# Performance work log

Hardware: AMD Instinct MI355X
Metric: run time of the kernel (lower is better)

## Reference

```python
import jax, jax.numpy as jnp
import numpy as np

B, C, H, W = 32, 3, 128, 128
OH, OW = 32, 32
N = OH * OW


def calc_mask(mu_x, mu_y, sigma_x, sigma_y):
    # Gaussian receptive-field mask, normalized per neuron over (C,H,W) and
    # rescaled by sqrt(C*H*W), as in AdaptiveLocal2DLayer.calc_U (channel_separate=False,
    # normed=True). The mask is identical across channels, so we keep it [H,W,N]
    # and fold the channel count C into the normalization.
    xg = jnp.linspace(0.0, 1.0, W)
    yg = jnp.linspace(0.0, 1.0, H)
    gx = jnp.exp(-0.5 * ((xg[:, None] - mu_x[None, :]) / sigma_x[None, :]) ** 2)  # [W,N]
    gy = jnp.exp(-0.5 * ((yg[:, None] - mu_y[None, :]) / sigma_y[None, :]) ** 2)  # [H,N]
    g = gy[:, None, :] * gx[None, :, :]  # [H,W,N]
    sumsq = C * jnp.sum(g * g, axis=(0, 1), keepdims=True)  # per-neuron sum over C,H,W
    return g / jnp.sqrt(sumsq) * jnp.sqrt(jnp.asarray(C * H * W, dtype=g.dtype))


def setup_inputs() -> dict:
    key = jax.random.key(0)
    kx, kw = jax.random.split(key)
    x = jax.random.normal(kx, (B, C, H, W), dtype=jnp.float32)
    # mu_init='spread': grid of centers with margin 0.2 (np.meshgrid default 'xy')
    margin = 0.2
    grid_y, grid_x = jnp.meshgrid(
        jnp.linspace(margin, 1.0 - margin, OH),
        jnp.linspace(margin, 1.0 - margin, OW),
        indexing='xy')
    mu_x = grid_x.flatten().astype(jnp.float32)
    mu_y = grid_y.flatten().astype(jnp.float32)
    sigma_x = jnp.full((N,), 0.1, dtype=jnp.float32)
    sigma_y = jnp.full((N,), 0.1, dtype=jnp.float32)
    # weight init as in the module: uniform(-bound, bound) with
    # bound = gain*sqrt(6/(eff_fan_in + fan_out)), eff_fan_in = sum(mask^2)
    mask = calc_mask(mu_x, mu_y, sigma_x, sigma_y)
    eff_fan_in = C * jnp.sum(mask ** 2)
    gain = float(np.sqrt(2.0))  # calculate_gain('relu')
    bound = gain * jnp.sqrt(6.0 / (eff_fan_in + N))
    weights = jax.random.uniform(kw, (C, H, W, N), minval=-bound, maxval=bound,
                                 dtype=jnp.float32)
    return {"x": x, "mu_x": mu_x, "mu_y": mu_y,
            "sigma_x": sigma_x, "sigma_y": sigma_y, "weights": weights}


def reference(x, mu_x, mu_y, sigma_x, sigma_y, weights):
    # forward: weighted_mask = mask * weights; tensordot over (C,H,W)
    mask = calc_mask(mu_x, mu_y, sigma_x, sigma_y)  # [H,W,N]
    wm = mask[None, :, :, :] * weights               # [C,H,W,N]
    out = jnp.einsum('bchw,chwn->bn', x, wm)         # [B,N]
    return out.reshape(x.shape[0], 1, OH, OW)
```

## Files before the change

kernel.cpp:

```cpp
#include <hip/hip_runtime.h>

#define BB 32
#define CC 3
#define HH 128
#define WW 128
#define NN 1024
#define KK (CC*HH*WW)
#define NROWS (CC*HH)
#define KSR NROWS
#define BH 16
#define NSL 512
#define WCH 4
#define NCH (WW/WCH)
#define SG 8
#define STEP (1.0f/127.0f)

__global__ void scale_kernel(const float* __restrict__ mu_x,
                             const float* __restrict__ mu_y,
                             const float* __restrict__ sigma_x,
                             const float* __restrict__ sigma_y,
                             float* __restrict__ scale) {
    int n = blockIdx.x * blockDim.x + threadIdx.x;
    if (n >= NN) return;
    float mux = mu_x[n], muy = mu_y[n];
    float isx = 1.0f / sigma_x[n], isy = 1.0f / sigma_y[n];
    float Sx = 0.f, Sy = 0.f;
    for (int i = 0; i < WW; ++i) {
        float dx = (i * STEP - mux) * isx;
        Sx += __expf(-dx * dx);
        float dy = (i * STEP - muy) * isy;
        Sy += __expf(-dy * dy);
    }
    scale[n] = sqrtf((float)(HH * WW) / (Sx * Sy));
}

__global__ void xpose_kernel(const float* __restrict__ x, float* __restrict__ xT) {
    __shared__ float tile[64][BB + 1];
    int k0 = blockIdx.x * 64;
    int lane = threadIdx.x & 63;
    int bgrp = threadIdx.x >> 6;
#pragma unroll
    for (int i = 0; i < 8; ++i) {
        int b = bgrp * 8 + i;
        tile[lane][b] = x[(size_t)b * KK + k0 + lane];
    }
    __syncthreads();
    int b = threadIdx.x & 31;
    int kk0 = threadIdx.x >> 5;
#pragma unroll
    for (int i = 0; i < 8; ++i) {
        int kk = i * 8 + kk0;
        xT[(size_t)(k0 + kk) * BB + b] = tile[kk][b];
    }
}

__global__ __launch_bounds__(256) void main_pipe(
    const float* __restrict__ weights,
    const float* __restrict__ xT,
    const float* __restrict__ scale,
    const float* __restrict__ mu_x, const float* __restrict__ mu_y,
    const float* __restrict__ sigma_x, const float* __restrict__ sigma_y,
    float* __restrict__ part)
{
    const int tid = threadIdx.x;

    const int d    = blockIdx.x;
    const int xcd  = d & 7;
    const int slot = d >> 3;
    const int g    = xcd * (KSR / 8) + (slot >> 2);
    const int sib  = slot & 3;
    const int b0   = (sib & 1) * BH;
    const int nh   = sib >> 1;
    const int r    = g;
    const int h    = r & (HH - 1);
    const int np   = nh * 256 + tid;

    const float2 mux2 = ((const float2*)mu_x)[np];
    const float2 sx2  = ((const float2*)sigma_x)[np];
    const float2 muy2 = ((const float2*)mu_y)[np];
    const float2 sy2  = ((const float2*)sigma_y)[np];
    const float2 sc2  = ((const float2*)scale)[np];

    float mux[2] = {mux2.x, mux2.y};
    float ax[2], axs[2], Bf[2], gyrow[2];
    ax[0] = -0.5f/(sx2.x*sx2.x); ax[1] = -0.5f/(sx2.y*sx2.y);
    axs[0] = ax[0]*STEP;         axs[1] = ax[1]*STEP;
    Bf[0] = __expf(2.f*axs[0]*STEP); Bf[1] = __expf(2.f*axs[1]*STEP);
    {
        const float hp = h * STEP;
        float ayc, dd;
        ayc = -0.5f/(sy2.x*sy2.x); dd = hp-muy2.x; gyrow[0] = __expf(ayc*dd*dd)*sc2.x;
        ayc = -0.5f/(sy2.y*sy2.y); dd = hp-muy2.y; gyrow[1] = __expf(ayc*dd*dd)*sc2.y;
    }

    const float* wbase = weights + (size_t)r * WW * NN + np * 2;
    const float4* xr4  = (const float4*)xT + (size_t)r * (WW * BB / 4) + (b0 >> 2);

    float2 wR[2][4];
#define WLOAD(BUF, C)                                                   \
    {                                                                   \
        _Pragma("unroll")                                               \
        for (int i = 0; i < 4; ++i)                                     \
            wR[BUF][i] = *(const float2*)(wbase + (size_t)((C)*WCH + i) * NN); \
    }

    float2 acc[BH];
#pragma unroll
    for (int b = 0; b < BH; ++b) acc[b] = make_float2(0.f, 0.f);

    float g2[2], r2[2];
    auto resync = [&](int w0) {
        const float w0s = (float)w0 * STEP;
#pragma unroll
        for (int j = 0; j < 2; ++j) {
            const float dd = w0s - mux[j];
            g2[j] = __expf(ax[j] * dd * dd) * gyrow[j];
            r2[j] = __expf(axs[j] * (2.f * dd + STEP));
        }
    };

#define FMAQ(XC, B)                                                     \
    {                                                                   \
        acc[B].x = fmaf(XC, t0, acc[B].x);                              \
        acc[B].y = fmaf(XC, t1, acc[B].y);                              \
    }

#define CHUNK(BUF, C)                                                   \
    {                                                                   \
        if (((C) & 3) == 0) resync((C) * WCH);                          \
        _Pragma("unroll")                                               \
        for (int i = 0; i < 4; ++i) {                                   \
            const int w = (C) * WCH + i;                                \
            const float4 xq0 = xr4[w*8 + 0];                            \
            const float4 xq1 = xr4[w*8 + 1];                            \
            const float4 xq2 = xr4[w*8 + 2];                            \
            const float4 xq3 = xr4[w*8 + 3];                            \
            const float t0 = g2[0] * wR[BUF][i].x;                      \
            const float t1 = g2[1] * wR[BUF][i].y;                      \
            FMAQ(xq0.x,  0) FMAQ(xq0.y,  1) FMAQ(xq0.z,  2) FMAQ(xq0.w,  3) \
            FMAQ(xq1.x,  4) FMAQ(xq1.y,  5) FMAQ(xq1.z,  6) FMAQ(xq1.w,  7) \
            FMAQ(xq2.x,  8) FMAQ(xq2.y,  9) FMAQ(xq2.z, 10) FMAQ(xq2.w, 11) \
            FMAQ(xq3.x, 12) FMAQ(xq3.y, 13) FMAQ(xq3.z, 14) FMAQ(xq3.w, 15) \
            g2[0] *= r2[0]; g2[1] *= r2[1];                             \
            r2[0] *= Bf[0]; r2[1] *= Bf[1];                             \
        }                                                               \
    }

    WLOAD(0, 0);
    for (int c = 0; c < NCH; c += 2) {
        WLOAD(1, c + 1);
        CHUNK(0, c);
        if (c + 2 < NCH) WLOAD(0, c + 2);
        CHUNK(1, c + 1);
    }
#undef CHUNK
#undef FMAQ
#undef WLOAD

    float* pp = part + ((size_t)g * BB + b0) * NN + np * 2;
#pragma unroll
    for (int b = 0; b < BH; ++b)
        *(float2*)(pp + (size_t)b * NN) = acc[b];
}

__global__ __launch_bounds__(256) void reduce1_kernel(const float* __restrict__ part,
                                                      float* __restrict__ part2) {
    const int sg = blockIdx.x >> 5;
    const int cq = (blockIdx.x & 31) * 256 + threadIdx.x;
    const int s0 = sg * (KSR / SG);
    float4 a = make_float4(0.f, 0.f, 0.f, 0.f);
#pragma unroll 4
    for (int s = 0; s < KSR / SG; ++s) {
        const float4 v = *(const float4*)(part + (size_t)(s0 + s) * (BB * NN) + cq * 4);
        a.x += v.x; a.y += v.y; a.z += v.z; a.w += v.w;
    }
    *(float4*)(part2 + ((size_t)sg * (BB * NN) + cq * 4)) = a;
}

__global__ __launch_bounds__(256) void reduce2_kernel(const float* __restrict__ part2,
                                                      float* __restrict__ out) {
    const int cq = blockIdx.x * 256 + threadIdx.x;
    float4 a = make_float4(0.f, 0.f, 0.f, 0.f);
#pragma unroll
    for (int sgi = 0; sgi < SG; ++sgi) {
        const float4 v = *(const float4*)(part2 + (size_t)sgi * (BB * NN) + cq * 4);
        a.x += v.x; a.y += v.y; a.z += v.z; a.w += v.w;
    }
    *(float4*)(out + cq * 4) = a;
}

__global__ __launch_bounds__(256) void main_fallback(
    const float* __restrict__ weights,
    const float* __restrict__ x,
    const float* __restrict__ mu_x, const float* __restrict__ mu_y,
    const float* __restrict__ sigma_x, const float* __restrict__ sigma_y,
    float* __restrict__ dst)
{
    __shared__ float tile[2][WW][8];
    const int tid = threadIdx.x;
    const int g   = blockIdx.x;
    const int b0  = blockIdx.y * 8;
    const int r0  = g * 2;

    {
        const int b = tid & 7;
        const int c = tid >> 3;
        const float* xp = x + (size_t)(b0 + b) * KK + (size_t)r0 * WW + c * 8;
        const float4 v0 = ((const float4*)xp)[0];
        const float4 v1 = ((const float4*)xp)[1];
        const int row = (c * 8) >> 7;
        const int w   = (c * 8) & (WW - 1);
        tile[row][w+0][b] = v0.x; tile[row][w+1][b] = v0.y;
        tile[row][w+2][b] = v0.z; tile[row][w+3][b] = v0.w;
        tile[row][w+4][b] = v1.x; tile[row][w+5][b] = v1.y;
        tile[row][w+6][b] = v1.z; tile[row][w+7][b] = v1.w;
    }

    float4 mux4 = ((const float4*)mu_x)[tid];
    float4 muy4 = ((const float4*)mu_y)[tid];
    float4 sx4  = ((const float4*)sigma_x)[tid];
    float4 sy4  = ((const float4*)sigma_y)[tid];
    float4 ax4, ay4, sc4;
    ax4.x=-0.5f/(sx4.x*sx4.x); ax4.y=-0.5f/(sx4.y*sx4.y);
    ax4.z=-0.5f/(sx4.z*sx4.z); ax4.w=-0.5f/(sx4.w*sx4.w);
    ay4.x=-0.5f/(sy4.x*sy4.x); ay4.y=-0.5f/(sy4.y*sy4.y);
    ay4.z=-0.5f/(sy4.z*sy4.z); ay4.w=-0.5f/(sy4.w*sy4.w);
    {
        float Sx[4]={0,0,0,0}, Sy[4]={0,0,0,0};
        for (int i = 0; i < WW; ++i) {
            float pp = i * STEP, dd;
            dd=pp-mux4.x; Sx[0]+=__expf(2.f*ax4.x*dd*dd);
            dd=pp-mux4.y; Sx[1]+=__expf(2.f*ax4.y*dd*dd);
            dd=pp-mux4.z; Sx[2]+=__expf(2.f*ax4.z*dd*dd);
            dd=pp-mux4.w; Sx[3]+=__expf(2.f*ax4.w*dd*dd);
            dd=pp-muy4.x; Sy[0]+=__expf(2.f*ay4.x*dd*dd);
            dd=pp-muy4.y; Sy[1]+=__expf(2.f*ay4.y*dd*dd);
            dd=pp-muy4.z; Sy[2]+=__expf(2.f*ay4.z*dd*dd);
            dd=pp-muy4.w; Sy[3]+=__expf(2.f*ay4.w*dd*dd);
        }
        sc4.x = sqrtf((float)(HH*WW)/(Sx[0]*Sy[0]));
        sc4.y = sqrtf((float)(HH*WW)/(Sx[1]*Sy[1]));
        sc4.z = sqrtf((float)(HH*WW)/(Sx[2]*Sy[2]));
        sc4.w = sqrtf((float)(HH*WW)/(Sx[3]*Sy[3]));
    }
    __syncthreads();

    float acc[8][4];
#pragma unroll
    for (int b = 0; b < 8; ++b)
        acc[b][0] = acc[b][1] = acc[b][2] = acc[b][3] = 0.f;

#pragma unroll
    for (int rr = 0; rr < 2; ++rr) {
        const int rrow = r0 + rr;
        const int hh = rrow & (HH - 1);
        float4 gys;
        {
            float hp = hh * STEP, dd;
            dd=hp-muy4.x; gys.x = __expf(ay4.x*dd*dd) * sc4.x;
            dd=hp-muy4.y; gys.y = __expf(ay4.y*dd*dd) * sc4.y;
            dd=hp-muy4.z; gys.z = __expf(ay4.z*dd*dd) * sc4.z;
            dd=hp-muy4.w; gys.w = __expf(ay4.w*dd*dd) * sc4.w;
        }
        const float4* wp = (const float4*)(weights + (size_t)rrow * WW * NN) + tid;
        float racc[8][4];
#pragma unroll
        for (int b = 0; b < 8; ++b)
            racc[b][0] = racc[b][1] = racc[b][2] = racc[b][3] = 0.f;
        for (int w = 0; w < WW; ++w) {
            const float4 wt = wp[(size_t)w * (NN/4)];
            float pp = w * STEP, dd;
            float4 t;
            dd=pp-mux4.x; t.x = __expf(ax4.x*dd*dd) * wt.x;
            dd=pp-mux4.y; t.y = __expf(ax4.y*dd*dd) * wt.y;
            dd=pp-mux4.z; t.z = __expf(ax4.z*dd*dd) * wt.z;
            dd=pp-mux4.w; t.w = __expf(ax4.w*dd*dd) * wt.w;
            const float4* trp = (const float4*)&tile[rr][w][0];
            float xs[8];
            ((float4*)xs)[0] = trp[0]; ((float4*)xs)[1] = trp[1];
#pragma unroll
            for (int b = 0; b < 8; ++b) {
                racc[b][0] = fmaf(xs[b], t.x, racc[b][0]);
                racc[b][1] = fmaf(xs[b], t.y, racc[b][1]);
                racc[b][2] = fmaf(xs[b], t.z, racc[b][2]);
                racc[b][3] = fmaf(xs[b], t.w, racc[b][3]);
            }
        }
#pragma unroll
        for (int b = 0; b < 8; ++b) {
            acc[b][0] = fmaf(gys.x, racc[b][0], acc[b][0]);
            acc[b][1] = fmaf(gys.y, racc[b][1], acc[b][1]);
            acc[b][2] = fmaf(gys.z, racc[b][2], acc[b][2]);
            acc[b][3] = fmaf(gys.w, racc[b][3], acc[b][3]);
        }
    }

    float* op = dst + (size_t)b0 * NN + tid * 4;
#pragma unroll
    for (int b = 0; b < 8; ++b) {
        atomicAdd(op + (size_t)b * NN + 0, acc[b][0]);
        atomicAdd(op + (size_t)b * NN + 1, acc[b][1]);
        atomicAdd(op + (size_t)b * NN + 2, acc[b][2]);
        atomicAdd(op + (size_t)b * NN + 3, acc[b][3]);
    }
}

extern "C" void kernel_launch(void* const* d_in, const int* in_sizes, int n_in,
                              void* d_out, int out_size, void* d_ws, size_t ws_size,
                              hipStream_t stream) {
    const float* x       = (const float*)d_in[0];
    const float* mu_x    = (const float*)d_in[1];
    const float* mu_y    = (const float*)d_in[2];
    const float* sigma_x = (const float*)d_in[3];
    const float* sigma_y = (const float*)d_in[4];
    const float* weights = (const float*)d_in[5];
    float* out = (float*)d_out;

    float* scale = (float*)d_ws;
    float* xT    = (float*)((char*)d_ws + 4096);
    float* part  = xT + (size_t)KK * BB;
    float* part2 = part + (size_t)KSR * BB * NN;
    const size_t need = 4096 +
        sizeof(float) * ((size_t)KK * BB + (size_t)KSR * BB * NN + (size_t)SG * BB * NN);

    if (ws_size >= need) {
        scale_kernel<<<(NN + 255) / 256, 256, 0, stream>>>(mu_x, mu_y, sigma_x, sigma_y, scale);
        xpose_kernel<<<KK / 64, 256, 0, stream>>>(x, xT);
        main_pipe<<<KSR * 4, 256, 0, stream>>>(weights, xT, scale,
                                               mu_x, mu_y, sigma_x, sigma_y, part);
        reduce1_kernel<<<32 * SG, 256, 0, stream>>>(part, part2);
        reduce2_kernel<<<BB * NN / 4 / 256, 256, 0, stream>>>(part2, out);
    } else {
        hipMemsetAsync(d_out, 0, (size_t)out_size * sizeof(float), stream);
        dim3 grid(NROWS / 2, 4);
        main_fallback<<<grid, 256, 0, stream>>>(weights, x,
                                                mu_x, mu_y, sigma_x, sigma_y, out);
    }
}
```

Before: 76.97 us.

## Process all 32 batches per block to halve weight reads in main pipe

Each main_pipe block now accumulates all 32 batch rows instead of 16, so the grid shrinks from 4 to 2 blocks per input row. Every weight element is then loaded once instead of twice, cutting traffic on the weight tensor that dominates the kernel's memory reads. The cost is 64 accumulator registers per thread instead of 32, which can lower occupancy, and fewer blocks to hide latency.

Result: slower. 89.08 us (+15.7%).

```diff
diff --git a/kernel.cpp b/kernel.cpp
--- a/kernel.cpp
+++ b/kernel.cpp
@@ -8,8 +8,6 @@
 #define KK (CC*HH*WW)
 #define NROWS (CC*HH)
 #define KSR NROWS
-#define BH 16
-#define NSL 512
 #define WCH 4
 #define NCH (WW/WCH)
 #define SG 8
@@ -67,11 +65,8 @@
     const int d    = blockIdx.x;
     const int xcd  = d & 7;
     const int slot = d >> 3;
-    const int g    = xcd * (KSR / 8) + (slot >> 2);
-    const int sib  = slot & 3;
-    const int b0   = (sib & 1) * BH;
-    const int nh   = sib >> 1;
-    const int r    = g;
+    const int r    = xcd * (NROWS / 8) + (slot >> 1);
+    const int nh   = slot & 1;
     const int h    = r & (HH - 1);
     const int np   = nh * 256 + tid;
 
@@ -88,13 +83,13 @@
     Bf[0] = __expf(2.f*axs[0]*STEP); Bf[1] = __expf(2.f*axs[1]*STEP);
     {
         const float hp = h * STEP;
-        float ayc, dd;
-        ayc = -0.5f/(sy2.x*sy2.x); dd = hp-muy2.x; gyrow[0] = __expf(ayc*dd*dd)*sc2.x;
-        ayc = -0.5f/(sy2.y*sy2.y); dd = hp-muy2.y; gyrow[1] = __expf(ayc*dd*dd)*sc2.y;
+        float dd;
+        dd = hp - muy2.x; gyrow[0] = __expf(-0.5f/(sy2.x*sy2.x)*dd*dd) * sc2.x;
+        dd = hp - muy2.y; gyrow[1] = __expf(-0.5f/(sy2.y*sy2.y)*dd*dd) * sc2.y;
     }
 
     const float* wbase = weights + (size_t)r * WW * NN + np * 2;
-    const float4* xr4  = (const float4*)xT + (size_t)r * (WW * BB / 4) + (b0 >> 2);
+    const float4* xr4  = (const float4*)xT + (size_t)r * (WW * BB / 4);
 
     float2 wR[2][4];
 #define WLOAD(BUF, C)                                                   \
@@ -104,9 +99,9 @@
             wR[BUF][i] = *(const float2*)(wbase + (size_t)((C)*WCH + i) * NN); \
     }
 
-    float2 acc[BH];
-#pragma unroll
-    for (int b = 0; b < BH; ++b) acc[b] = make_float2(0.f, 0.f);
+    float2 acc[BB];
+#pragma unroll
+    for (int b = 0; b < BB; ++b) acc[b] = make_float2(0.f, 0.f);
 
     float g2[2], r2[2];
     auto resync = [&](int w0) {
@@ -123,6 +118,13 @@
     {                                                                   \
         acc[B].x = fmaf(XC, t0, acc[B].x);                              \
         acc[B].y = fmaf(XC, t1, acc[B].y);                              \
+    }
+
+#define XSTEP(Q, W)                                                     \
+    {                                                                   \
+        const float4 xq = xr4[(W)*8 + (Q)];                             \
+        FMAQ(xq.x, 4*(Q)+0) FMAQ(xq.y, 4*(Q)+1)                         \
+        FMAQ(xq.z, 4*(Q)+2) FMAQ(xq.w, 4*(Q)+3)                         \
     }
 
 #define CHUNK(BUF, C)                                                   \
@@ -131,16 +133,10 @@
         _Pragma("unroll")                                               \
         for (int i = 0; i < 4; ++i) {                                   \
             const int w = (C) * WCH + i;                                \
-            const float4 xq0 = xr4[w*8 + 0];                            \
-            const float4 xq1 = xr4[w*8 + 1];                            \
-            const float4 xq2 = xr4[w*8 + 2];                            \
-            const float4 xq3 = xr4[w*8 + 3];                            \
             const float t0 = g2[0] * wR[BUF][i].x;                      \
             const float t1 = g2[1] * wR[BUF][i].y;                      \
-            FMAQ(xq0.x,  0) FMAQ(xq0.y,  1) FMAQ(xq0.z,  2) FMAQ(xq0.w,  3) \
-            FMAQ(xq1.x,  4) FMAQ(xq1.y,  5) FMAQ(xq1.z,  6) FMAQ(xq1.w,  7) \
-            FMAQ(xq2.x,  8) FMAQ(xq2.y,  9) FMAQ(xq2.z, 10) FMAQ(xq2.w, 11) \
-            FMAQ(xq3.x, 12) FMAQ(xq3.y, 13) FMAQ(xq3.z, 14) FMAQ(xq3.w, 15) \
+            XSTEP(0, w) XSTEP(1, w) XSTEP(2, w) XSTEP(3, w)             \
+            XSTEP(4, w) XSTEP(5, w) XSTEP(6, w) XSTEP(7, w)             \
             g2[0] *= r2[0]; g2[1] *= r2[1];                             \
             r2[0] *= Bf[0]; r2[1] *= Bf[1];                             \
         }                                                               \
@@ -154,12 +150,13 @@
         CHUNK(1, c + 1);
     }
 #undef CHUNK
+#undef XSTEP
 #undef FMAQ
 #undef WLOAD
 
-    float* pp = part + ((size_t)g * BB + b0) * NN + np * 2;
-#pragma unroll
-    for (int b = 0; b < BH; ++b)
+    float* pp = part + ((size_t)r * BB) * NN + np * 2;
+#pragma unroll
+    for (int b = 0; b < BB; ++b)
         *(float2*)(pp + (size_t)b * NN) = acc[b];
 }
 
@@ -326,8 +323,8 @@
     if (ws_size >= need) {
         scale_kernel<<<(NN + 255) / 256, 256, 0, stream>>>(mu_x, mu_y, sigma_x, sigma_y, scale);
         xpose_kernel<<<KK / 64, 256, 0, stream>>>(x, xT);
-        main_pipe<<<KSR * 4, 256, 0, stream>>>(weights, xT, scale,
-                                               mu_x, mu_y, sigma_x, sigma_y, part);
+        main_pipe<<<NROWS * 2, 256, 0, stream>>>(weights, xT, scale,
+                                                 mu_x, mu_y, sigma_x, sigma_y, part);
         reduce1_kernel<<<32 * SG, 256, 0, stream>>>(part, part2);
         reduce2_kernel<<<BB * NN / 4 / 256, 256, 0, stream>>>(part2, out);
     } else {
```
